# Kernel optimization log

Measured on AMD Instinct MI355X. Metric: run time of the kernel, lower is better.

## Reference

```python
import jax, jax.numpy as jnp
import numpy as np

B, T, CIN, CH, SZ = 4, 6, 3, 64, 128
KS = [3, 5, 7]


def _conv(x, w, b, pad):
    # x: [N,Ci,H,W], w: [Co,Ci,k,k]
    y = jax.lax.conv_general_dilated(
        x, w, window_strides=(1, 1), padding=[(pad, pad), (pad, pad)],
        dimension_numbers=('NCHW', 'OIHW', 'NCHW'))
    return y + b[None, :, None, None]


def setup_inputs() -> dict:
    key = jax.random.key(0)
    ks = jax.random.split(key, 16)
    inp = {}
    inp['x'] = jax.random.normal(ks[0], (B, T, CIN, SZ, SZ), jnp.float32)
    for i in range(3):
        inp[f'h{i}'] = jnp.zeros((B, CH, SZ, SZ), jnp.float32)
    # 1x1 projection conv
    inp['w1x1'] = jax.random.normal(ks[1], (CH, CIN, 1, 1), jnp.float32) / np.sqrt(CIN).astype(np.float32)
    inp['b1x1'] = jnp.zeros((CH,), jnp.float32)
    # 3 ConvGRU layers, gates: reset (r), update (u), out (o)
    ki = 2
    for i, k in enumerate(KS):
        cin = (CIN if i == 0 else CH) + CH  # concat(input, hidden)
        s = np.float32(1.0 / np.sqrt(cin * k * k))
        for g in ('r', 'u', 'o'):
            inp[f'w{g}{i}'] = jax.random.normal(ks[ki], (CH, cin, k, k), jnp.float32) * s
            inp[f'b{g}{i}'] = jnp.zeros((CH,), jnp.float32)
            ki += 1
    return inp


def _cell(inp, h, wr, br, wu, bu, wo, bo, k):
    pad = k // 2
    stacked = jnp.concatenate([inp, h], axis=1)
    u = jax.nn.sigmoid(_conv(stacked, wu, bu, pad))
    r = jax.nn.sigmoid(_conv(stacked, wr, br, pad))
    o = jnp.tanh(_conv(jnp.concatenate([inp, h * r], axis=1), wo, bo, pad))
    return h * (1.0 - u) + o * u


def reference(x, h0, h1, h2, w1x1, b1x1,
              wr0, br0, wu0, bu0, wo0, bo0,
              wr1, br1, wu1, bu1, wo1, bo1,
              wr2, br2, wu2, bu2, wo2, bo2):
    b, t, c, hh, ww = x.shape
    x0 = _conv(x.reshape(b * t, c, hh, ww), w1x1, b1x1, 0)  # [b*t, CH, H, W]
    layers = [(wr0, br0, wu0, bu0, wo0, bo0, 3),
              (wr1, br1, wu1, bu1, wo1, bo1, 5),
              (wr2, br2, wu2, bu2, wo2, bo2, 7)]

    def step(carry, xt):
        hs = list(carry)
        layer_in = xt
        new_hs = []
        for i, (wr, br, wu, bu, wo, bo, k) in enumerate(layers):
            hn = _cell(layer_in, hs[i], wr, br, wu, bu, wo, bo, k)
            new_hs.append(hn)
            layer_in = hn
        return tuple(new_hs), None

    xs = jnp.transpose(x, (1, 0, 2, 3, 4))  # [t,b,c,H,W]
    (h0f, h1f, h2f), _ = jax.lax.scan(step, (h0, h1, h2), xs)
    # original returns ((x0, hidden[-1]), hidden); flattened here
    return (x0, h0f, h1f, h2f)
```

## Files before the change

### kernel.cpp

```cpp
#include <hip/hip_runtime.h>
#include <math.h>

constexpr int Bn  = 4;
constexpr int T   = 6;
constexpr int CIN = 3;
constexpr int CH  = 64;
constexpr int IMG = 128;
constexpr int HW  = IMG * IMG;

constexpr int CLY = 136;
constexpr long CLN = 4L * CLY * CLY * 64;
constexpr long CLNX = 4L * CLY * CLY * 32;

typedef short bf16x8 __attribute__((ext_vector_type(8)));
typedef float f32x4  __attribute__((ext_vector_type(4)));

__device__ __forceinline__ unsigned short f2bf(float f) {
    union { float f; unsigned int u; } v; v.f = f;
    unsigned int u = v.u;
    unsigned int r = (u + 0x7FFFu + ((u >> 16) & 1u)) >> 16;
    return (unsigned short)r;
}
__device__ __forceinline__ float bf2f(unsigned short s) {
    union { unsigned int u; float f; } v; v.u = ((unsigned int)s) << 16;
    return v.f;
}
__device__ __forceinline__ float sigmoidf_(float v) { return 1.f / (1.f + __expf(-v)); }
__device__ __forceinline__ float tanhf_(float v)    { return 1.f - 2.f / (1.f + __expf(2.f * v)); }

__global__ void xform_w(const float* __restrict__ wA, const float* __restrict__ wB,
                        unsigned short* __restrict__ dst,
                        int K, int C0, int NCIC, int NG) {
    int idx   = blockIdx.x * 256 + threadIdx.x;
    int total = NG * K * K * NCIC * 4 * 64;
    if (idx >= total) return;
    int CI   = C0 + 64;
    int KK   = K * K;
    int lane = idx & 63;
    int rest = idx >> 6;
    int c    = rest & 3; rest >>= 2;
    int cic  = rest % NCIC; rest /= NCIC;
    int kyx  = rest % KK;
    int cog  = rest / KK;
    const float* w = cog ? wB : wA;
    int co = c * 16 + (lane & 15);
    union { unsigned short u[8]; uint4 q; } t;
    #pragma unroll
    for (int j = 0; j < 8; ++j) {
        int ci_new = cic * 32 + ((lane >> 4) * 8) + j;
        int ci_o   = (ci_new < 64) ? (C0 + ci_new) : (ci_new - 64);
        bool valid = (ci_new < 64) || (ci_new - 64 < C0);
        float f = valid ? w[((long)co * CI + ci_o) * KK + kyx] : 0.f;
        t.u[j] = f2bf(f);
    }
    *(uint4*)(dst + (long)(idx >> 6) * 8 * 64 + lane * 8) = t.q;
}

__global__ void build_cl(const float* __restrict__ src, long bstride, int C0,
                         unsigned short* __restrict__ dst, int NG, int CST) {
    int i    = blockIdx.x * 256 + threadIdx.x;
    int px   = i & 16383;
    int rest = i >> 14;
    int g    = rest % NG;
    int b    = rest / NG;
    int y    = px >> 7, x = px & 127;
    union { unsigned short u[8]; uint4 q; } t;
    #pragma unroll
    for (int j = 0; j < 8; ++j) {
        int ci  = g * 8 + j;
        float f = (ci < C0) ? src[(long)b * bstride + (long)ci * HW + px] : 0.f;
        t.u[j] = f2bf(f);
    }
    long off = (((long)b * CLY + 4 + y) * CLY + 4 + x) * CST + g * 8;
    *(uint4*)(dst + off) = t.q;
}

__global__ void unpack_h(const unsigned short* __restrict__ clh, float* __restrict__ H) {
    int i  = blockIdx.x * 256 + threadIdx.x;
    int b  = i >> 14, px = i & 16383;
    int y  = px >> 7, x = px & 127;
    const unsigned short* p = clh + (((long)b * CLY + 4 + y) * CLY + 4 + x) * 64;
    float* Hb = H + (long)b * 64 * HW + px;
    #pragma unroll
    for (int g = 0; g < 8; ++g) {
        union { unsigned short us[8]; uint4 q; } t;
        t.q = *(const uint4*)(p + g * 8);
        #pragma unroll
        for (int j = 0; j < 8; ++j)
            Hb[(long)(g * 8 + j) * HW] = bf2f(t.us[j]);
    }
}

template<int K, int NCIC, int S, int MODE, int CST>
__global__ __launch_bounds__(256)
void conv_l0(const unsigned short* __restrict__ clh,
             const unsigned short* __restrict__ clin,
             const unsigned short* __restrict__ wt,
             const float* __restrict__ bias_a,
             const float* __restrict__ bias_b,
             unsigned short* __restrict__ ubuf,
             unsigned short* __restrict__ clh2,
             unsigned short* __restrict__ clhL)
{
    constexpr int HOFF = 4 - K / 2;
    constexpr int KK   = K * K;
    constexpr int NF   = NCIC * 4;
    __shared__ unsigned short alds[2][NF * 512];

    int w    = threadIdx.x >> 6;
    int lane = threadIdx.x & 63;
    int cog  = (MODE == 0) ? blockIdx.y : 0;
    int m    = blockIdx.x;
    int k8   = m & 7;
    int q    = m >> 3;
    int b    = k8 >> 1;
    int y, x0;
    if (S == 4) { y = (k8 & 1) * 64 + (q >> 1) * 4 + w; x0 = (q & 1) * 64; }
    else        { y = (k8 & 1) * 64 + (q >> 2) * 4 + w; x0 = (q & 3) * 32; }
    int n  = lane & 15;
    int kg = lane >> 4;

    f32x4 acc[4][S];
    #pragma unroll
    for (int c = 0; c < 4; ++c)
        #pragma unroll
        for (int s = 0; s < S; ++s)
            acc[c][s] = (f32x4){0.f, 0.f, 0.f, 0.f};

    long rbh = ((long)(b * CLY + HOFF + y) * CLY + HOFF + x0 + n) * 64 + kg * 8;
    long rbi = ((long)(b * CLY + HOFF + y) * CLY + HOFF + x0 + n) * CST + kg * 8;
    const unsigned short* wcog = wt + (long)cog * KK * NF * 512;

    #define STAGEW(bi, kyx_) do {                                              \
        const unsigned short* _src = wcog + (long)(kyx_) * NF * 512;           \
        _Pragma("unroll")                                                      \
        for (int j = 0; j < NCIC; ++j) {                                       \
            int f = j * 4 + w;                                                 \
            __builtin_amdgcn_global_load_lds(                                  \
                (const __attribute__((address_space(1))) void*)(_src + f * 512 + lane * 8), \
                (__attribute__((address_space(3))) void*)(&alds[bi][f * 512]), \
                16, 0, 0);                                                     \
        }                                                                      \
    } while (0)

    STAGEW(0, 0);
    int cur = 0;
    for (int kyx = 0; kyx < KK; ++kyx) {
        if (kyx + 1 < KK) {
            STAGEW(cur ^ 1, kyx + 1);
            asm volatile("s_waitcnt vmcnt(%0)" :: "n"(NCIC) : "memory");
        } else {
            asm volatile("s_waitcnt vmcnt(0)" ::: "memory");
        }
        __builtin_amdgcn_s_barrier();
        asm volatile("" ::: "memory");

        int ky = kyx / K;
        int kx = kyx - ky * K;
        long offh = rbh + (long)(ky * CLY + kx) * 64;
        long offi = rbi + (long)(ky * CLY + kx) * CST;
        #pragma unroll
        for (int cic = 0; cic < NCIC; ++cic) {
            bf16x8 bfr[S], afr[4];
            #pragma unroll
            for (int s = 0; s < S; ++s) {
                if (cic < 2) bfr[s] = *(const bf16x8*)(clh  + offh + s * 16 * 64  + cic * 32);
                else         bfr[s] = *(const bf16x8*)(clin + offi + s * 16 * CST + (cic - 2) * 32);
            }
            #pragma unroll
            for (int c = 0; c < 4; ++c)
                afr[c] = *(const bf16x8*)(&alds[cur][(cic * 4 + c) * 512 + lane * 8]);
            #pragma unroll
            for (int c = 0; c < 4; ++c)
                #pragma unroll
                for (int s = 0; s < S; ++s)
                    acc[c][s] = __builtin_amdgcn_mfma_f32_16x16x32_bf16(afr[c], bfr[s], acc[c][s], 0, 0, 0);
        }
        asm volatile("" ::: "memory");
        __builtin_amdgcn_s_barrier();
        cur ^= 1;
    }
    #undef STAGEW

    #pragma unroll
    for (int coc = 0; coc < 4; ++coc) {
        int co_l = coc * 16 + kg * 4;
        #pragma unroll
        for (int s = 0; s < S; ++s) {
            int x = x0 + s * 16 + n;
            f32x4 v = acc[coc][s];
            long cloff = (((long)b * CLY + 4 + y) * CLY + 4 + x) * 64 + co_l;
            if (MODE == 0) {
                if (cog == 0) {
                    union { unsigned short us[4]; unsigned long long d; } t;
                    #pragma unroll
                    for (int rr = 0; rr < 4; ++rr)
                        t.us[rr] = f2bf(sigmoidf_(v[rr] + bias_a[co_l + rr]));
                    *(unsigned long long*)(ubuf + (((long)b * HW + y * IMG + x) * 64 + co_l)) = t.d;
                } else {
                    union { unsigned short us[4]; unsigned long long d; } hh, t;
                    hh.d = *(const unsigned long long*)(clh + cloff);
                    #pragma unroll
                    for (int rr = 0; rr < 4; ++rr) {
                        float rv = sigmoidf_(v[rr] + bias_b[co_l + rr]);
                        t.us[rr] = f2bf(bf2f(hh.us[rr]) * rv);
                    }
                    *(unsigned long long*)(clh2 + cloff) = t.d;
                }
            } else {
                union { unsigned short us[4]; unsigned long long d; } uu, hh, t;
                uu.d = *(const unsigned long long*)(ubuf + (((long)b * HW + y * IMG + x) * 64 + co_l));
                hh.d = *(const unsigned long long*)(clhL + cloff);
                #pragma unroll
                for (int rr = 0; rr < 4; ++rr) {
                    float o  = tanhf_(v[rr] + bias_a[co_l + rr]);
                    float hv = bf2f(hh.us[rr]);
                    float uv = bf2f(uu.us[rr]);
                    t.us[rr] = f2bf(hv + uv * (o - hv));
                }
                *(unsigned long long*)(clhL + cloff) = t.d;
            }
        }
    }
}

template<int K, int MODE>
__global__ __launch_bounds__(512)
void conv_db(const unsigned short* __restrict__ clh,
             const unsigned short* __restrict__ clin,
             const unsigned short* __restrict__ wt,
             const float* __restrict__ bias_a,
             const float* __restrict__ bias_b,
             unsigned short* __restrict__ ubuf,
             unsigned short* __restrict__ clh2,
             unsigned short* __restrict__ clhL)
{
    constexpr int HOFF = 4 - K / 2;
    constexpr int KK   = K * K;
    constexpr int ROWS = K + 3;
    constexpr int PXT  = 31 + K;
    constexpr int SUBT = ROWS * PXT;
    constexpr int SUBTP = (SUBT + 7) & ~7;
    constexpr int NCHUNK = 4 * SUBTP;
    constexpr int NGRP = NCHUNK / 64;
    constexpr int VCNT = NGRP / 8;
    constexpr int NCW = (MODE == 0) ? 2 : 1;

    __shared__ __align__(16) unsigned char tile[2][NCHUNK * 16];

    int tid  = threadIdx.x;
    int w    = tid >> 6;
    int lane = tid & 63;
    int cog  = (MODE == 0) ? (w >> 2) : 0;
    int cb   = (MODE == 0) ? ((w >> 1) & 1) * 2 : (w >> 1);
    int rp   = w & 1;
    int m    = blockIdx.x;
    int k8   = m & 7;
    int t8   = m >> 3;
    int b    = k8 >> 1;
    int y0   = (k8 & 1) * 64 + (t8 >> 2) * 4;
    int x0   = (t8 & 3) * 32;
    int n    = lane & 15;
    int kg   = lane >> 4;

    f32x4 acc[NCW][2][2];
    #pragma unroll
    for (int c = 0; c < NCW; ++c)
        #pragma unroll
        for (int rr = 0; rr < 2; ++rr)
            #pragma unroll
            for (int s = 0; s < 2; ++s)
                acc[c][rr][s] = (f32x4){0.f, 0.f, 0.f, 0.f};

    const unsigned short* wbase = wt + (long)cog * KK * 16 * 512;

    #define STAGE(bi, ph_) do {                                                \
        const unsigned short* sp_ = ((ph_) < 2) ? clh : clin;                  \
        int half_ = ((ph_) & 1) * 32;                                          \
        _Pragma("unroll 1")                                                    \
        for (int g = w; g < NGRP; g += 8) {                                    \
            int c_  = g * 64 + lane;                                           \
            int cg  = c_ / SUBTP;                                              \
            int rem = c_ - cg * SUBTP;                                         \
            int r   = rem / PXT;                                               \
            int px  = rem - r * PXT;                                           \
            const unsigned short* src_ = sp_ +                                 \
                (((long)(b * CLY + HOFF + y0 + r)) * CLY + (HOFF + x0 + px)) * 64 \
                + half_ + cg * 8;                                              \
            __builtin_amdgcn_global_load_lds(                                  \
                (const __attribute__((address_space(1))) void*)src_,           \
                (__attribute__((address_space(3))) void*)(&tile[bi][g * 64 * 16]), \
                16, 0, 0);                                                     \
        }                                                                      \
    } while (0)

    int cur = 0;
    STAGE(0, 0);
    #pragma unroll 1
    for (int ph = 0; ph < 4; ++ph) {
        if (ph < 3) {
            STAGE(cur ^ 1, ph + 1);
            asm volatile("s_waitcnt vmcnt(%0)" :: "n"(VCNT) : "memory");
        } else {
            asm volatile("s_waitcnt vmcnt(0)" ::: "memory");
        }
        __builtin_amdgcn_s_barrier();
        asm volatile("" ::: "memory");

        const unsigned char* tb = tile[cur];
        #pragma unroll 1
        for (int ky = 0; ky < K; ++ky) {
            const unsigned char* row0 = tb + (kg * SUBTP + (rp * 2 + 0 + ky) * PXT) * 16;
            const unsigned char* row1 = tb + (kg * SUBTP + (rp * 2 + 1 + ky) * PXT) * 16;
            #pragma unroll
            for (int kx = 0; kx < K; ++kx) {
                bf16x8 bv[2][2];
                #pragma unroll
                for (int s = 0; s < 2; ++s) {
                    bv[0][s] = *(const bf16x8*)(row0 + (kx + s * 16 + n) * 16);
                    bv[1][s] = *(const bf16x8*)(row1 + (kx + s * 16 + n) * 16);
                }
                const unsigned short* wk = wbase
                    + ((long)((ky * K + kx) * 4 + ph) * 4 + cb) * 512 + lane * 8;
                #pragma unroll
                for (int c = 0; c < NCW; ++c) {
                    bf16x8 av = *(const bf16x8*)(wk + c * 512);
                    #pragma unroll
                    for (int rr = 0; rr < 2; ++rr)
                        #pragma unroll
                        for (int s = 0; s < 2; ++s)
                            acc[c][rr][s] = __builtin_amdgcn_mfma_f32_16x16x32_bf16(av, bv[rr][s], acc[c][rr][s], 0, 0, 0);
                }
            }
        }
        asm volatile("" ::: "memory");
        __builtin_amdgcn_s_barrier();
        cur ^= 1;
    }
    #undef STAGE

    #pragma unroll
    for (int c = 0; c < NCW; ++c) {
        int co_l = (cb + c) * 16 + kg * 4;
        #pragma unroll
        for (int rr = 0; rr < 2; ++rr) {
            int yy = y0 + rp * 2 + rr;
            #pragma unroll
            for (int s = 0; s < 2; ++s) {
                int xx = x0 + s * 16 + n;
                f32x4 v = acc[c][rr][s];
                long cloff = (((long)b * CLY + 4 + yy) * CLY + 4 + xx) * 64 + co_l;
                if (MODE == 0) {
                    if (cog == 0) {
                        union { unsigned short us[4]; unsigned long long d; } t;
                        #pragma unroll
                        for (int q4 = 0; q4 < 4; ++q4)
                            t.us[q4] = f2bf(sigmoidf_(v[q4] + bias_a[co_l + q4]));
                        *(unsigned long long*)(ubuf + (((long)b * HW + yy * IMG + xx) * 64 + co_l)) = t.d;
                    } else {
                        union { unsigned short us[4]; unsigned long long d; } hh, t;
                        hh.d = *(const unsigned long long*)(clh + cloff);
                        #pragma unroll
                        for (int q4 = 0; q4 < 4; ++q4) {
                            float rv = sigmoidf_(v[q4] + bias_b[co_l + q4]);
                            t.us[q4] = f2bf(bf2f(hh.us[q4]) * rv);
                        }
                        *(unsigned long long*)(clh2 + cloff) = t.d;
                    }
                } else {
                    union { unsigned short us[4]; unsigned long long d; } uu, hh, t;
                    uu.d = *(const unsigned long long*)(ubuf + (((long)b * HW + yy * IMG + xx) * 64 + co_l));
                    hh.d = *(const unsigned long long*)(clhL + cloff);
                    #pragma unroll
                    for (int q4 = 0; q4 < 4; ++q4) {
                        float o  = tanhf_(v[q4] + bias_a[co_l + q4]);
                        float hv = bf2f(hh.us[q4]);
                        float uv = bf2f(uu.us[q4]);
                        t.us[q4] = f2bf(hv + uv * (o - hv));
                    }
                    *(unsigned long long*)(clhL + cloff) = t.d;
                }
            }
        }
    }
}

__global__ void conv1x1(const float* __restrict__ x, const float* __restrict__ w,
                        const float* __restrict__ bias, float* __restrict__ out) {
    int i  = blockIdx.x * 256 + threadIdx.x;
    int q  = HW / 4;
    int p4 = i % q;
    int co = (i / q) & 63;
    int f  = i / (q * 64);
    const float4* xb = reinterpret_cast<const float4*>(x + (long)f * 3 * HW);
    float4 x0 = xb[p4];
    float4 x1 = xb[p4 + q];
    float4 x2 = xb[p4 + 2 * q];
    float w0 = w[co * 3], w1 = w[co * 3 + 1], w2 = w[co * 3 + 2];
    float bv = bias[co];
    float4 o;
    o.x = bv + x0.x * w0 + x1.x * w1 + x2.x * w2;
    o.y = bv + x0.y * w0 + x1.y * w1 + x2.y * w2;
    o.z = bv + x0.z * w0 + x1.z * w1 + x2.z * w2;
    o.w = bv + x0.w * w0 + x1.w * w1 + x2.w * w2;
    reinterpret_cast<float4*>(out)[i] = o;
}

extern "C" void kernel_launch(void* const* d_in, const int* in_sizes, int n_in,
                              void* d_out, int out_size, void* d_ws, size_t ws_size,
                              hipStream_t stream) {
    (void)in_sizes; (void)n_in; (void)out_size; (void)d_ws; (void)ws_size;

    const float* x  = (const float*)d_in[0];
    const float* w1 = (const float*)d_in[4];
    const float* b1 = (const float*)d_in[5];

    float* out = (float*)d_out;

    const long X0_N = 24L * CH * HW;
    const long HN   = (long)Bn * CH * HW;

    float* H[3] = { out + X0_N, out + X0_N + HN, out + X0_N + 2 * HN };

    unsigned short* sc    = (unsigned short*)out;
    unsigned short* ubuf  = sc;
    unsigned short* CLH0  = sc + 4194304;
    unsigned short* CLH1  = CLH0 + CLN;
    unsigned short* CLH2  = CLH1 + CLN;
    unsigned short* clh2  = CLH2 + CLN;
    unsigned short* clinx = clh2 + CLN;
    unsigned short* wt    = clinx + CLNX;

    const long WT_UR[3] = { 0,      165888, 780288  };
    const long WT_O [3] = { 110592, 575488, 1583104 };

    const int Ks[3]   = { 3, 5, 7 };
    const int C0s[3]  = { CIN, CH, CH };
    const int NCIC[3] = { 3, 4, 4 };

    hipMemsetAsync(CLH0, 0, (4 * CLN + CLNX) * sizeof(unsigned short), stream);

    for (int L = 0; L < 3; ++L) {
        const float* wr = (const float*)d_in[6 + 6 * L];
        const float* wu = (const float*)d_in[8 + 6 * L];
        const float* wo = (const float*)d_in[10 + 6 * L];
        int K = Ks[L], C0 = C0s[L], NC = NCIC[L];
        int tot_ur = 2 * K * K * NC * 4 * 64;
        int tot_o  = 1 * K * K * NC * 4 * 64;
        xform_w<<<(tot_ur + 255) / 256, 256, 0, stream>>>(wu, wr, wt + WT_UR[L], K, C0, NC, 2);
        xform_w<<<(tot_o  + 255) / 256, 256, 0, stream>>>(wo, wo, wt + WT_O[L],  K, C0, NC, 1);
    }

    unsigned short* CLH[3] = { CLH0, CLH1, CLH2 };
    for (int L = 0; L < 3; ++L)
        build_cl<<<4 * 8 * 64, 256, 0, stream>>>((const float*)d_in[1 + L],
                                                 (long)CH * HW, 64, CLH[L], 8, 64);

    for (int t = 0; t < T; ++t) {
        build_cl<<<4 * 4 * 64, 256, 0, stream>>>(x + (long)t * CIN * HW,
                                                 (long)T * CIN * HW, CIN, clinx, 4, 32);
        {
            const float* br = (const float*)d_in[7];
            const float* bu = (const float*)d_in[9];
            const float* bo = (const float*)d_in[11];
            conv_l0<3, 3, 4, 0, 32><<<dim3(256, 2), 256, 0, stream>>>(
                CLH0, clinx, wt + WT_UR[0], bu, br, ubuf, clh2, nullptr);
            conv_l0<3, 3, 2, 1, 32><<<dim3(512, 1), 256, 0, stream>>>(
                clh2, clinx, wt + WT_O[0], bo, nullptr, ubuf, nullptr, CLH0);
        }
        {
            const float* br = (const float*)d_in[13];
            const float* bu = (const float*)d_in[15];
            const float* bo = (const float*)d_in[17];
            conv_db<5, 0><<<512, 512, 0, stream>>>(
                CLH1, CLH0, wt + WT_UR[1], bu, br, ubuf, clh2, nullptr);
            conv_db<5, 1><<<512, 512, 0, stream>>>(
                clh2, CLH0, wt + WT_O[1], bo, nullptr, ubuf, nullptr, CLH1);
        }
        {
            const float* br = (const float*)d_in[19];
            const float* bu = (const float*)d_in[21];
            const float* bo = (const float*)d_in[23];
            conv_db<7, 0><<<512, 512, 0, stream>>>(
                CLH2, CLH1, wt + WT_UR[2], bu, br, ubuf, clh2, nullptr);
            conv_db<7, 1><<<512, 512, 0, stream>>>(
                clh2, CLH1, wt + WT_O[2], bo, nullptr, ubuf, nullptr, CLH2);
        }
    }

    for (int L = 0; L < 3; ++L)
        unpack_h<<<256, 256, 0, stream>>>(CLH[L], H[L]);

    conv1x1<<<(24 * CH * HW / 4 + 255) / 256, 256, 0, stream>>>(x, w1, b1, out);
}
```

Before: 2.045 ms.

## Use 32x32x16 MFMA conv kernel for layer 1-2 update/reset gates

Adds a new conv32 kernel for the update and reset gates of layers 1 and 2. It uses 32x32x16 bf16 MFMA with a 16-float accumulator, tiles of 2 rows by 32 pixels, and a double-buffered LDS pipeline fed by global_load_lds over four 32-channel phases. A matching weight-layout transform (xform_w32) is added, and the grid doubles to 1024 blocks with launch_bounds occupancy hint 6. The aim is higher MFMA throughput and more input reuse per LDS load. The cost is a smaller tile, so more halo overhead, and weights are read directly from global memory inside the inner loop.

```diff
diff --git a/kernel.cpp b/kernel.cpp
--- a/kernel.cpp
+++ b/kernel.cpp
@@ -14,6 +14,7 @@
 
 typedef short bf16x8 __attribute__((ext_vector_type(8)));
 typedef float f32x4  __attribute__((ext_vector_type(4)));
+typedef float f32x16 __attribute__((ext_vector_type(16)));
 
 __device__ __forceinline__ unsigned short f2bf(float f) {
     union { float f; unsigned int u; } v; v.f = f;
@@ -54,6 +55,33 @@
         t.u[j] = f2bf(f);
     }
     *(uint4*)(dst + (long)(idx >> 6) * 8 * 64 + lane * 8) = t.q;
+}
+
+__global__ void xform_w32(const float* __restrict__ wA, const float* __restrict__ wB,
+                          unsigned short* __restrict__ dst, int K, int C0) {
+    int KK    = K * K;
+    int total = 2 * KK * 16 * 64;
+    int idx   = blockIdx.x * 256 + threadIdx.x;
+    if (idx >= total) return;
+    int CI   = C0 + 64;
+    int lane = idx & 63;
+    int rest = idx >> 6;
+    int sub  = rest & 3; rest >>= 2;
+    int ph   = rest & 3; rest >>= 2;
+    int kyx  = rest % KK;
+    int cog  = rest / KK;
+    const float* w = cog ? wB : wA;
+    int co = (sub >> 1) * 32 + (lane & 31);
+    union { unsigned short u[8]; uint4 q; } t;
+    #pragma unroll
+    for (int j = 0; j < 8; ++j) {
+        int ci_new = ph * 32 + (sub & 1) * 16 + ((lane >> 5) * 8) + j;
+        int ci_o   = (ci_new < 64) ? (C0 + ci_new) : (ci_new - 64);
+        bool valid = (ci_new < 64) || (ci_new - 64 < C0);
+        float f = valid ? w[((long)co * CI + ci_o) * KK + kyx] : 0.f;
+        t.u[j] = f2bf(f);
+    }
+    *(uint4*)(dst + (long)(idx >> 6) * 512 + lane * 8) = t.q;
 }
 
 __global__ void build_cl(const float* __restrict__ src, long bstride, int C0,
@@ -220,6 +248,133 @@
                 }
                 *(unsigned long long*)(clhL + cloff) = t.d;
             }
+        }
+    }
+}
+
+template<int K>
+__global__ __launch_bounds__(512, 6)
+void conv32(const unsigned short* __restrict__ clh,
+            const unsigned short* __restrict__ clin,
+            const unsigned short* __restrict__ wt,
+            const float* __restrict__ bias_u,
+            const float* __restrict__ bias_r,
+            unsigned short* __restrict__ ubuf,
+            unsigned short* __restrict__ clh2)
+{
+    constexpr int HOFF  = 4 - K / 2;
+    constexpr int KK    = K * K;
+    constexpr int ROWS  = K + 1;
+    constexpr int PXT   = 31 + K;
+    constexpr int SUBT  = ROWS * PXT;
+    constexpr int SUBTP = (SUBT + 15) & ~15;
+    constexpr int NCHUNK = 4 * SUBTP;
+    constexpr int NGRP  = NCHUNK / 64;
+    constexpr int VCNT  = NGRP / 8;
+
+    __shared__ __align__(16) unsigned char tile[2][NCHUNK * 16];
+
+    int tid    = threadIdx.x;
+    int w      = tid >> 6;
+    int lane   = tid & 63;
+    int gate   = w >> 2;
+    int cohalf = (w >> 1) & 1;
+    int row    = w & 1;
+    int m      = blockIdx.x;
+    int k8     = m & 7;
+    int t8     = m >> 3;
+    int b      = k8 >> 1;
+    int y0     = (k8 & 1) * 64 + (t8 >> 2) * 2;
+    int x0     = (t8 & 3) * 32;
+    int pxl    = lane & 31;
+    int kh     = lane >> 5;
+
+    f32x16 acc;
+    #pragma unroll
+    for (int i = 0; i < 16; ++i) acc[i] = 0.f;
+
+    const unsigned short* wbase = wt + (long)gate * KK * 16 * 512;
+
+    #define STAGE(bi, ph_) do {                                                \
+        const unsigned short* sp_ = ((ph_) < 2) ? clh : clin;                  \
+        int half_ = ((ph_) & 1) * 32;                                          \
+        _Pragma("unroll 1")                                                    \
+        for (int g = w; g < NGRP; g += 8) {                                    \
+            int c_  = g * 64 + lane;                                           \
+            int cg  = c_ / SUBTP;                                              \
+            int rem = c_ - cg * SUBTP;                                         \
+            int r   = rem / PXT;                                               \
+            int px  = rem - r * PXT;                                           \
+            const unsigned short* src_ = sp_ +                                 \
+                (((long)(b * CLY + HOFF + y0 + r)) * CLY + (HOFF + x0 + px)) * 64 \
+                + half_ + cg * 8;                                              \
+            __builtin_amdgcn_global_load_lds(                                  \
+                (const __attribute__((address_space(1))) void*)src_,           \
+                (__attribute__((address_space(3))) void*)(&tile[bi][g * 64 * 16]), \
+                16, 0, 0);                                                     \
+        }                                                                      \
+    } while (0)
+
+    int cur = 0;
+    STAGE(0, 0);
+    #pragma unroll 1
+    for (int ph = 0; ph < 4; ++ph) {
+        if (ph < 3) {
+            STAGE(cur ^ 1, ph + 1);
+            asm volatile("s_waitcnt vmcnt(%0)" :: "n"(VCNT) : "memory");
+        } else {
+            asm volatile("s_waitcnt vmcnt(0)" ::: "memory");
+        }
+        __builtin_amdgcn_s_barrier();
+        asm volatile("" ::: "memory");
+
+        const unsigned char* tb = tile[cur];
+        #pragma unroll 1
+        for (int ky = 0; ky < K; ++ky) {
+            const unsigned char* rb0 = tb + ((kh)     * SUBTP + (row + ky) * PXT + pxl) * 16;
+            const unsigned char* rb1 = tb + ((2 + kh) * SUBTP + (row + ky) * PXT + pxl) * 16;
+            #pragma unroll
+            for (int kx = 0; kx < K; ++kx) {
+                bf16x8 b0 = *(const bf16x8*)(rb0 + kx * 16);
+                bf16x8 b1 = *(const bf16x8*)(rb1 + kx * 16);
+                const unsigned short* wk = wbase
+                    + ((long)((ky * K + kx) * 4 + ph) * 4 + cohalf * 2) * 512 + lane * 8;
+                bf16x8 a0 = *(const bf16x8*)(wk);
+                bf16x8 a1 = *(const bf16x8*)(wk + 512);
+                acc = __builtin_amdgcn_mfma_f32_32x32x16_bf16(a0, b0, acc, 0, 0, 0);
+                acc = __builtin_amdgcn_mfma_f32_32x32x16_bf16(a1, b1, acc, 0, 0, 0);
+            }
+        }
+        asm volatile("" ::: "memory");
+        __builtin_amdgcn_s_barrier();
+        cur ^= 1;
+    }
+    #undef STAGE
+
+    int yy = y0 + row;
+    int xx = x0 + pxl;
+    const float* bias = gate ? bias_r : bias_u;
+    #pragma unroll
+    for (int q = 0; q < 4; ++q) {
+        int co0 = cohalf * 32 + kh * 4 + q * 8;
+        float v0 = acc[4 * q + 0], v1 = acc[4 * q + 1];
+        float v2 = acc[4 * q + 2], v3 = acc[4 * q + 3];
+        if (gate == 0) {
+            union { unsigned short us[4]; unsigned long long d; } t;
+            t.us[0] = f2bf(sigmoidf_(v0 + bias[co0 + 0]));
+            t.us[1] = f2bf(sigmoidf_(v1 + bias[co0 + 1]));
+            t.us[2] = f2bf(sigmoidf_(v2 + bias[co0 + 2]));
+            t.us[3] = f2bf(sigmoidf_(v3 + bias[co0 + 3]));
+            *(unsigned long long*)(ubuf + (((long)b * HW + yy * IMG + xx) * 64 + co0)) = t.d;
+        } else {
+            long cloff = (((long)b * CLY + 4 + yy) * CLY + 4 + xx) * 64 + co0;
+            union { unsigned short us[4]; unsigned long long d; } hh, t;
+            hh.d = *(const unsigned long long*)(clh + cloff);
+            t.us[0] = f2bf(bf2f(hh.us[0]) * sigmoidf_(v0 + bias[co0 + 0]));
+            t.us[1] = f2bf(bf2f(hh.us[1]) * sigmoidf_(v1 + bias[co0 + 1]));
+            t.us[2] = f2bf(bf2f(hh.us[2]) * sigmoidf_(v2 + bias[co0 + 2]));
+            t.us[3] = f2bf(bf2f(hh.us[3]) * sigmoidf_(v3 + bias[co0 + 3]));
+            *(unsigned long long*)(clh2 + cloff) = t.d;
         }
     }
 }
@@ -447,8 +602,11 @@
         int K = Ks[L], C0 = C0s[L], NC = NCIC[L];
         int tot_ur = 2 * K * K * NC * 4 * 64;
         int tot_o  = 1 * K * K * NC * 4 * 64;
-        xform_w<<<(tot_ur + 255) / 256, 256, 0, stream>>>(wu, wr, wt + WT_UR[L], K, C0, NC, 2);
-        xform_w<<<(tot_o  + 255) / 256, 256, 0, stream>>>(wo, wo, wt + WT_O[L],  K, C0, NC, 1);
+        if (L == 0)
+            xform_w<<<(tot_ur + 255) / 256, 256, 0, stream>>>(wu, wr, wt + WT_UR[L], K, C0, NC, 2);
+        else
+            xform_w32<<<(tot_ur + 255) / 256, 256, 0, stream>>>(wu, wr, wt + WT_UR[L], K, C0);
+        xform_w<<<(tot_o + 255) / 256, 256, 0, stream>>>(wo, wo, wt + WT_O[L], K, C0, NC, 1);
     }
 
     unsigned short* CLH[3] = { CLH0, CLH1, CLH2 };
@@ -472,8 +630,8 @@
             const float* br = (const float*)d_in[13];
             const float* bu = (const float*)d_in[15];
             const float* bo = (const float*)d_in[17];
-            conv_db<5, 0><<<512, 512, 0, stream>>>(
-                CLH1, CLH0, wt + WT_UR[1], bu, br, ubuf, clh2, nullptr);
+            conv32<5><<<1024, 512, 0, stream>>>(
+                CLH1, CLH0, wt + WT_UR[1], bu, br, ubuf, clh2);
             conv_db<5, 1><<<512, 512, 0, stream>>>(
                 clh2, CLH0, wt + WT_O[1], bo, nullptr, ubuf, nullptr, CLH1);
         }
@@ -481,8 +639,8 @@
             const float* br = (const float*)d_in[19];
             const float* bu = (const float*)d_in[21];
             const float* bo = (const float*)d_in[23];
-            conv_db<7, 0><<<512, 512, 0, stream>>>(
-                CLH2, CLH1, wt + WT_UR[2], bu, br, ubuf, clh2, nullptr);
+            conv32<7><<<1024, 512, 0, stream>>>(
+                CLH2, CLH1, wt + WT_UR[2], bu, br, ubuf, clh2);
             conv_db<7, 1><<<512, 512, 0, stream>>>(
                 clh2, CLH1, wt + WT_O[2], bo, nullptr, ubuf, nullptr, CLH2);
         }
```

After: 2.316 ms. +13.3%, slower.
